# Optimization experiments

Hardware: AMD Instinct MI355X
Metric: run time of the kernel (lower is better)

The kernel has to match this reference:

```python
import jax, jax.numpy as jnp
import numpy as np

CLASS_DIM = 4   # hardcoded in DsFunction1
PROTO_DIM = 20  # hardcoded in DsFunction1


def setup_inputs() -> dict:
    key = jax.random.key(0)
    k1, k2, k3 = jax.random.split(key, 3)
    B, C, H, Wd, D = 2, 16, 64, 64, 64
    inp = jax.random.normal(k1, (B, C, H, Wd, D), dtype=jnp.float32)
    W = jax.random.normal(k2, (PROTO_DIM, C), dtype=jnp.float32)
    BETA = jax.random.normal(k3, (PROTO_DIM, CLASS_DIM), dtype=jnp.float32) * 0.5
    alpha = jnp.zeros((PROTO_DIM, 1), dtype=jnp.float32)           # init 0 per reset_parameters
    gamma = jnp.full((PROTO_DIM, 1), 0.1, dtype=jnp.float32)       # init 0.1 per reset_parameters
    return {"input": inp, "W": W, "BETA": BETA, "alpha": alpha, "gamma": gamma}


def _ds_forward(x, W, BETA, alpha, gamma):
    # x: [B,C,H,Wd,D]; W: [K,C]; BETA: [K,M]; alpha, gamma: [K,1]
    B, C, H, Wd, D = x.shape
    BETA2 = BETA * BETA
    U = BETA2 / jnp.sum(BETA2, axis=1, keepdims=True)              # [K,M] membership weights
    alphap = 0.99 / (1.0 + jnp.exp(-alpha[:, 0]))                  # [K]

    # squared distances to prototypes: d[k] = 0.5 * ||x - W_k||^2 over channel dim
    x2 = jnp.sum(x * x, axis=1)                                    # [B,H,Wd,D]
    xw = jnp.einsum('bchwd,kc->kbhwd', x, W)                       # [K,B,H,Wd,D]
    w2 = jnp.sum(W * W, axis=1)                                    # [K]
    d = 0.5 * (x2[None] - 2.0 * xw + w2[:, None, None, None, None])  # [K,B,H,Wd,D]

    g2 = (gamma[:, 0] ** 2)[:, None, None, None, None]
    s = alphap[:, None, None, None, None] * jnp.exp(-g2 * d)       # [K,B,H,Wd,D]

    mfoc = U[:, :, None, None, None, None] * s[:, None]            # [K,M,B,H,Wd,D] focal masses
    momega = 1.0 - s                                               # [K,B,H,Wd,D] mass on Omega

    # sequential Dempster (unnormalized conjunctive) combination over prototypes
    def step(carry, km):
        mk_f, mk_o = carry                                         # [M,B,H,Wd,D], [B,H,Wd,D]
        m_f, m_o = km
        new_f = mk_f * (m_f + m_o[None]) + m_f * mk_o[None]
        new_o = mk_o * m_o
        return (new_f, new_o), None

    init = (jnp.zeros((CLASS_DIM, B, H, Wd, D), x.dtype),
            jnp.ones((B, H, Wd, D), x.dtype))
    (mk_f, mk_o), _ = jax.lax.scan(step, init, (mfoc, momega))

    mk = jnp.concatenate([mk_f, mk_o[None]], axis=0)               # [M+1,B,H,Wd,D]
    mk_n = mk / jnp.sum(mk, axis=0, keepdims=True)                 # normalize masses
    return jnp.transpose(mk_n, (1, 0, 2, 3, 4))                    # [B,M+1,H,Wd,D]


def reference(input, W, BETA, alpha, gamma):
    return _ds_forward(input, W, BETA, alpha, gamma)
```

## Files before the change

kernel.cpp:

```cpp
#include <hip/hip_runtime.h>
#include <hip/hip_bf16.h>
#include <math.h>

#define NK 20
#define NC 16
#define NM 4
#define TSTEP 2

typedef __attribute__((ext_vector_type(8)))  short  short8;
typedef __attribute__((ext_vector_type(16))) float  floatx16;

static __device__ __forceinline__ short bf16b(float f) {
    __hip_bfloat16 h = __float2bfloat16(f);
    return *reinterpret_cast<short*>(&h);
}

__global__ __launch_bounds__(256, 4) void ds_fused(
    const float* __restrict__ inp,
    const float* __restrict__ Wg,
    const float* __restrict__ BETAg,
    const float* __restrict__ alphag,
    const float* __restrict__ gammag,
    float* __restrict__ out,
    int S,
    int BS)
{
    __shared__ __align__(16) float sCst[32][8];
    __shared__ __align__(16) short sWpb[32][16];
    __shared__ short sNh[32];

    const int t = threadIdx.x;

    if (t < 32) {
        #pragma unroll
        for (int i = 0; i < 8; ++i) sCst[t][i] = 0.f;
        #pragma unroll
        for (int c = 0; c < NC; ++c) sWpb[t][c] = 0;
        sNh[t] = 0;
    }
    __syncthreads();
    if (t < NK) {
        const float L   = 1.4426950408889634f;
        const float g   = gammag[t];
        const float g2L = g * g * L;
        const int tm  = (t < 10) ? t : (t - 10);
        const int row = (tm & 3) + 8 * (tm >> 2) + ((t < 10) ? 0 : 4);
        float w2 = 0.f;
        #pragma unroll
        for (int c = 0; c < NC; ++c) {
            const float w = Wg[t*NC + c];
            sWpb[row][c] = bf16b(g2L * w);
            w2 = fmaf(w, w, w2);
        }
        const float nh = -0.5f * g2L;
        sNh[row] = bf16b(nh);
        const float p2nbk = exp2f(nh * w2);
        const float a  = 0.99f / (1.0f + __expf(-alphag[t]));
        const float ap = a * p2nbk;
        float b0 = BETAg[t*NM+0], b1 = BETAg[t*NM+1], b2 = BETAg[t*NM+2], b3 = BETAg[t*NM+3];
        b0 *= b0; b1 *= b1; b2 *= b2; b3 *= b3;
        const float uinv = 1.0f / (b0 + b1 + b2 + b3);
        sCst[row][0] = (1.0f - b0*uinv) * ap;
        sCst[row][1] = (1.0f - b1*uinv) * ap;
        sCst[row][2] = (1.0f - b2*uinv) * ap;
        sCst[row][3] = (1.0f - b3*uinv) * ap;
        sCst[row][4] = ap;
    }
    __syncthreads();

    const int lane = t & 63;
    const int half = lane >> 5;
    const int col  = lane & 31;
    const int gw   = blockIdx.x * 4 + (t >> 6);
    const int ebase = gw * (TSTEP * 32);

    const int b   = (ebase >= S) ? 1 : 0;
    const int spw = ebase - b * S;
    const float* xb0 = inp + (size_t)b * NC * S + spw + col;
    float xv[TSTEP][8];
    #pragma unroll
    for (int tt = 0; tt < TSTEP; ++tt)
        #pragma unroll
        for (int j = 0; j < 8; ++j)
            xv[tt][j] = xb0[(size_t)(8*half + j) * S + tt*32];

    const short8 afrag = *(const short8*)&sWpb[col][half*8];
    const short  nhb   = sNh[col];
    short8 nhfrag;
    #pragma unroll
    for (int j = 0; j < 8; ++j) nhfrag[j] = nhb;

    #pragma unroll
    for (int tt = 0; tt < TSTEP; ++tt) {
        const int sp = spw + tt*32 + col;

        short8 bfrag, b2frag;
        #pragma unroll
        for (int j = 0; j < 8; ++j) {
            const float v = xv[tt][j];
            bfrag[j]  = bf16b(v);
            b2frag[j] = bf16b(v * v);
        }

        floatx16 acc;
        #pragma unroll
        for (int i = 0; i < 16; ++i) acc[i] = 0.f;
        acc = __builtin_amdgcn_mfma_f32_32x32x16_bf16(afrag,  bfrag,  acc, 0, 0, 0);
        acc = __builtin_amdgcn_mfma_f32_32x32x16_bf16(nhfrag, b2frag, acc, 0, 0, 0);

        float P0 = 1.f, P1 = 1.f, P2 = 1.f, P3 = 1.f, PO = 1.f;
        #pragma unroll
        for (int r = 0; r < 10; ++r) {
            const int p = (r & 3) + 8*(r >> 2) + 4*half;
            const float4 cv = *(const float4*)&sCst[p][0];
            const float  aO = sCst[p][4];
            const float  ek = __builtin_amdgcn_exp2f(acc[r]);
            P0 *= fmaf(-cv.x, ek, 1.0f);
            P1 *= fmaf(-cv.y, ek, 1.0f);
            P2 *= fmaf(-cv.z, ek, 1.0f);
            P3 *= fmaf(-cv.w, ek, 1.0f);
            PO *= fmaf(-aO,   ek, 1.0f);
        }
        P0 *= __shfl_xor(P0, 32, 64);
        P1 *= __shfl_xor(P1, 32, 64);
        P2 *= __shfl_xor(P2, 32, 64);
        P3 *= __shfl_xor(P3, 32, 64);
        PO *= __shfl_xor(PO, 32, 64);

        const float O  = PO;
        const float f0 = P0 - O, f1 = P1 - O, f2 = P2 - O, f3 = P3 - O;
        const float inv = 1.0f / (f0 + f1 + f2 + f3 + O);

        float* op = out + (size_t)b * (NM+1) * S + sp;
        if (half == 0) {
            op[0]           = f0 * inv;
            op[(size_t)S]   = f1 * inv;
            op[(size_t)2*S] = f2 * inv;
        } else {
            op[(size_t)3*S] = f3 * inv;
            op[(size_t)4*S] = O  * inv;
        }
    }
}

extern "C" void kernel_launch(void* const* d_in, const int* in_sizes, int n_in,
                              void* d_out, int out_size, void* d_ws, size_t ws_size,
                              hipStream_t stream) {
    const float* inp   = (const float*)d_in[0];
    const float* Wg    = (const float*)d_in[1];
    const float* BETAg = (const float*)d_in[2];
    const float* alphag= (const float*)d_in[3];
    const float* gammag= (const float*)d_in[4];
    float* out = (float*)d_out;

    const int BS = in_sizes[0] / NC;
    const int S  = BS / 2;

    const int elems_per_block = 4 * TSTEP * 32;
    const int grid = (BS + elems_per_block - 1) / elems_per_block;
    ds_fused<<<grid, 256, 0, stream>>>(inp, Wg, BETAg, alphag, gammag, out, S, BS);
}
```

Measured before the change: 84.05 us.

## Double per-wave work and overlap input loads with prototype constant setup

Raises TSTEP from 2 to 4 so each wave handles 128 elements, halving the grid and the number of times the per-block setup is repeated. The input loads are now issued before the constant-table setup, so global memory latency overlaps that setup. The setup also writes each row directly by thread index and drops one barrier along with the separate zero-fill pass. The cost is higher register pressure from holding 32 loaded floats per thread, which may limit occupancy under the current launch bounds.

```diff
diff --git a/kernel.cpp b/kernel.cpp
--- a/kernel.cpp
+++ b/kernel.cpp
@@ -5,7 +5,7 @@
 #define NK 20
 #define NC 16
 #define NM 4
-#define TSTEP 2
+#define TSTEP 4
 
 typedef __attribute__((ext_vector_type(8)))  short  short8;
 typedef __attribute__((ext_vector_type(16))) float  floatx16;
@@ -30,44 +30,6 @@
     __shared__ short sNh[32];
 
     const int t = threadIdx.x;
-
-    if (t < 32) {
-        #pragma unroll
-        for (int i = 0; i < 8; ++i) sCst[t][i] = 0.f;
-        #pragma unroll
-        for (int c = 0; c < NC; ++c) sWpb[t][c] = 0;
-        sNh[t] = 0;
-    }
-    __syncthreads();
-    if (t < NK) {
-        const float L   = 1.4426950408889634f;
-        const float g   = gammag[t];
-        const float g2L = g * g * L;
-        const int tm  = (t < 10) ? t : (t - 10);
-        const int row = (tm & 3) + 8 * (tm >> 2) + ((t < 10) ? 0 : 4);
-        float w2 = 0.f;
-        #pragma unroll
-        for (int c = 0; c < NC; ++c) {
-            const float w = Wg[t*NC + c];
-            sWpb[row][c] = bf16b(g2L * w);
-            w2 = fmaf(w, w, w2);
-        }
-        const float nh = -0.5f * g2L;
-        sNh[row] = bf16b(nh);
-        const float p2nbk = exp2f(nh * w2);
-        const float a  = 0.99f / (1.0f + __expf(-alphag[t]));
-        const float ap = a * p2nbk;
-        float b0 = BETAg[t*NM+0], b1 = BETAg[t*NM+1], b2 = BETAg[t*NM+2], b3 = BETAg[t*NM+3];
-        b0 *= b0; b1 *= b1; b2 *= b2; b3 *= b3;
-        const float uinv = 1.0f / (b0 + b1 + b2 + b3);
-        sCst[row][0] = (1.0f - b0*uinv) * ap;
-        sCst[row][1] = (1.0f - b1*uinv) * ap;
-        sCst[row][2] = (1.0f - b2*uinv) * ap;
-        sCst[row][3] = (1.0f - b3*uinv) * ap;
-        sCst[row][4] = ap;
-    }
-    __syncthreads();
-
     const int lane = t & 63;
     const int half = lane >> 5;
     const int col  = lane & 31;
@@ -83,6 +45,46 @@
         #pragma unroll
         for (int j = 0; j < 8; ++j)
             xv[tt][j] = xb0[(size_t)(8*half + j) * S + tt*32];
+
+    if (t < 32) {
+        const int h   = (t >> 2) & 1;
+        const int tm  = (t & 3) + 4 * (t >> 3);
+        const bool live = (tm < 10);
+        if (live) {
+            const int k = tm + 10 * h;
+            const float L   = 1.4426950408889634f;
+            const float g   = gammag[k];
+            const float g2L = g * g * L;
+            float w2 = 0.f;
+            #pragma unroll
+            for (int c = 0; c < NC; ++c) {
+                const float w = Wg[k*NC + c];
+                sWpb[t][c] = bf16b(g2L * w);
+                w2 = fmaf(w, w, w2);
+            }
+            const float nh = -0.5f * g2L;
+            sNh[t] = bf16b(nh);
+            const float p2nbk = exp2f(nh * w2);
+            const float a  = 0.99f / (1.0f + __expf(-alphag[k]));
+            const float ap = a * p2nbk;
+            float b0 = BETAg[k*NM+0], b1 = BETAg[k*NM+1], b2 = BETAg[k*NM+2], b3 = BETAg[k*NM+3];
+            b0 *= b0; b1 *= b1; b2 *= b2; b3 *= b3;
+            const float uinv = 1.0f / (b0 + b1 + b2 + b3);
+            sCst[t][0] = (1.0f - b0*uinv) * ap;
+            sCst[t][1] = (1.0f - b1*uinv) * ap;
+            sCst[t][2] = (1.0f - b2*uinv) * ap;
+            sCst[t][3] = (1.0f - b3*uinv) * ap;
+            sCst[t][4] = ap;
+            sCst[t][5] = 0.f; sCst[t][6] = 0.f; sCst[t][7] = 0.f;
+        } else {
+            #pragma unroll
+            for (int i = 0; i < 8; ++i) sCst[t][i] = 0.f;
+            #pragma unroll
+            for (int c = 0; c < NC; ++c) sWpb[t][c] = 0;
+            sNh[t] = 0;
+        }
+    }
+    __syncthreads();
 
     const short8 afrag = *(const short8*)&sWpb[col][half*8];
     const short  nhb   = sNh[col];
```

Result: slower. 87.15 us (+3.7%).
